# Kernel optimization log

Hardware: AMD Instinct MI355X
Metric: run time of the kernel (lower is better)

## Reference

```python
import jax, jax.numpy as jnp
import numpy as np
import math

H = 16          # num heads
D = 64          # head dim
MAX_POS = 512   # max_position_embeddings


def setup_inputs() -> dict:
    key = jax.random.key(0)
    ks = jax.random.split(key, 8)
    B, S, E = 8, 512, 1024
    scale = 1.0 / math.sqrt(E)
    return {
        "hidden_states": jax.random.normal(ks[0], (B, S, E), jnp.float32),
        "attention_mask": jnp.zeros((B, 1, 1, S), jnp.float32),
        "Wq": jax.random.normal(ks[1], (E, E), jnp.float32) * scale,
        "bq": jnp.zeros((E,), jnp.float32),
        "Wk": jax.random.normal(ks[2], (E, E), jnp.float32) * scale,
        "bk": jnp.zeros((E,), jnp.float32),
        "Wv": jax.random.normal(ks[3], (E, E), jnp.float32) * scale,
        "bv": jnp.zeros((E,), jnp.float32),
        "dist_emb": jax.random.normal(ks[4], (2 * MAX_POS - 1, D), jnp.float32) * 0.02,
    }


def reference(hidden_states, attention_mask, Wq, bq, Wk, bk, Wv, bv, dist_emb):
    B, S, E = hidden_states.shape

    def heads(x):  # [B,S,E] -> [B,H,S,D]
        return x.reshape(B, S, H, D).transpose(0, 2, 1, 3)

    q = heads(hidden_states @ Wq + bq)
    k = heads(hidden_states @ Wk + bk)
    v = heads(hidden_states @ Wv + bv)

    # raw scores [B,H,S,S]
    scores = jnp.einsum('bhld,bhrd->bhlr', q, k)

    # relative position embedding lookup: distance[l,r] = l - r
    pos = jnp.arange(S)
    distance = pos[:, None] - pos[None, :]               # [S,S]
    pe = dist_emb[distance + MAX_POS - 1]                # [S,S,D]
    scores = scores + jnp.einsum('bhld,lrd->bhlr', q, pe)
    scores = scores + jnp.einsum('bhrd,lrd->bhlr', k, pe)

    scores = scores / math.sqrt(D) + attention_mask
    probs = jax.nn.softmax(scores, axis=-1)

    ctx = jnp.einsum('bhlr,bhrd->bhld', probs, v)        # [B,H,S,D]
    ctx = ctx.transpose(0, 2, 1, 3).reshape(B, S, H * D)
    return ctx
```

## Files before the change

kernel.cpp:

```cpp
#include <hip/hip_runtime.h>

#define BATCH 8
#define SEQ   512
#define EMB   1024
#define NH    16
#define HD    64

typedef __bf16 bf16x8 __attribute__((ext_vector_type(8)));
typedef float  f32x4  __attribute__((ext_vector_type(4)));

__device__ __forceinline__ unsigned short f2bf(float f){
  union { float f; unsigned u; } v; v.f = f;
  unsigned r = v.u + 0x7FFFu + ((v.u >> 16) & 1u);
  return (unsigned short)(r >> 16);
}
__device__ __forceinline__ unsigned short f2bfr(float f){
  union { float f; unsigned u; } v; v.f = f;
  return (unsigned short)((v.u + 0x8000u) >> 16);
}
__device__ __forceinline__ float bf2f(unsigned short s){
  union { unsigned u; float f; } v; v.u = ((unsigned)s) << 16;
  return v.f;
}

__device__ __forceinline__ float dpp_max16(float x){
  int t;
  t = __builtin_amdgcn_update_dpp(0, __builtin_bit_cast(int, x), 0xB1, 0xF, 0xF, true);
  x = fmaxf(x, __builtin_bit_cast(float, t));
  t = __builtin_amdgcn_update_dpp(0, __builtin_bit_cast(int, x), 0x4E, 0xF, 0xF, true);
  x = fmaxf(x, __builtin_bit_cast(float, t));
  t = __builtin_amdgcn_update_dpp(0, __builtin_bit_cast(int, x), 0x141, 0xF, 0xF, true);
  x = fmaxf(x, __builtin_bit_cast(float, t));
  t = __builtin_amdgcn_update_dpp(0, __builtin_bit_cast(int, x), 0x140, 0xF, 0xF, true);
  x = fmaxf(x, __builtin_bit_cast(float, t));
  return x;
}
__device__ __forceinline__ float dpp_sum16(float x){
  int t;
  t = __builtin_amdgcn_update_dpp(0, __builtin_bit_cast(int, x), 0xB1, 0xF, 0xF, true);
  x += __builtin_bit_cast(float, t);
  t = __builtin_amdgcn_update_dpp(0, __builtin_bit_cast(int, x), 0x4E, 0xF, 0xF, true);
  x += __builtin_bit_cast(float, t);
  t = __builtin_amdgcn_update_dpp(0, __builtin_bit_cast(int, x), 0x141, 0xF, 0xF, true);
  x += __builtin_bit_cast(float, t);
  t = __builtin_amdgcn_update_dpp(0, __builtin_bit_cast(int, x), 0x140, 0xF, 0xF, true);
  x += __builtin_bit_cast(float, t);
  return x;
}

__device__ __forceinline__ int swzc(int row, int chunk){
  return row * 128 + (((chunk ^ (row & 7)) & 7) << 4);
}
__device__ __forceinline__ int swz2(int row, int col){
  return row * 128 + ((((col >> 3) ^ (row & 7)) & 7) << 4) + ((col & 7) << 1);
}

__device__ __forceinline__ void gload16(const unsigned short* g, unsigned char* lds){
  __builtin_amdgcn_global_load_lds((const __attribute__((address_space(1))) unsigned int*)g,
                                   (__attribute__((address_space(3))) unsigned int*)lds,
                                   16, 0, 0);
}

__global__ void k_prep(const float* __restrict__ hid, unsigned short* __restrict__ hidb,
                       const float* __restrict__ dist, unsigned short* __restrict__ distb){
  int bid = blockIdx.x;
  if (bid < 4096){
    int i = (bid * 256 + threadIdx.x) * 4;
    float4 v = *(const float4*)(hid + i);
    ushort4 o; o.x = f2bf(v.x); o.y = f2bf(v.y); o.z = f2bf(v.z); o.w = f2bf(v.w);
    *(ushort4*)(hidb + i) = o;
  } else {
    int i = (bid - 4096) * 256 + threadIdx.x;
    distb[i] = (i < 1023 * 64) ? f2bf(dist[i]) : (unsigned short)0;
  }
}

__global__ void k_wt3(const float* __restrict__ Wq, const float* __restrict__ Wk,
                      const float* __restrict__ Wv, unsigned short* __restrict__ wqt,
                      unsigned short* __restrict__ wkt, unsigned short* __restrict__ wvt){
  const float* W = (blockIdx.z == 0) ? Wq : (blockIdx.z == 1) ? Wk : Wv;
  unsigned short* WT = (blockIdx.z == 0) ? wqt : (blockIdx.z == 1) ? wkt : wvt;
  __shared__ float t[32][33];
  int n0 = blockIdx.x * 32, k0 = blockIdx.y * 32;
  int tx = threadIdx.x, ty = threadIdx.y;
#pragma unroll
  for (int i = 0; i < 4; i++)
    t[ty + 8*i][tx] = W[(k0 + ty + 8*i) * EMB + n0 + tx];
  __syncthreads();
#pragma unroll
  for (int i = 0; i < 4; i++)
    WT[(n0 + ty + 8*i) * EMB + k0 + tx] = f2bf(t[tx][ty + 8*i]);
}

__global__ __launch_bounds__(256, 3) void k_gemm3(const unsigned short* __restrict__ A,
                                                  const unsigned short* __restrict__ wqt,
                                                  const unsigned short* __restrict__ wkt,
                                                  const unsigned short* __restrict__ wvt,
                                                  const float* __restrict__ bq,
                                                  const float* __restrict__ bk,
                                                  const float* __restrict__ bv,
                                                  unsigned short* __restrict__ qb,
                                                  unsigned short* __restrict__ kb,
                                                  unsigned short* __restrict__ vtb){
  int z = blockIdx.z;
  const unsigned short* BT = (z == 0) ? wqt : (z == 1) ? wkt : wvt;
  const float* bias = (z == 0) ? bq : (z == 1) ? bk : bv;
  unsigned short* out = (z == 0) ? qb : (z == 1) ? kb : vtb;
  int mode = (z == 2);

  __shared__ __align__(16) unsigned char sA[128 * 128];
  __shared__ __align__(16) unsigned char sB[128 * 128];
  int m0 = blockIdx.y * 128, n0 = blockIdx.x * 128;
  int t = threadIdx.x, w = t >> 6, lane = t & 63, g = lane >> 4, lr = lane & 15;
  int rowbase = (w >> 1) * 64, colbase = (w & 1) * 64;
  int lrow = lane >> 3, lc = lane & 7;
  f32x4 acc[4][4] = {};
  for (int k0 = 0; k0 < EMB; k0 += 64){
    __syncthreads();
#pragma unroll
    for (int i = 0; i < 4; i++){
      int row = (w + 4*i) * 8 + lrow;
      int cg  = lc ^ (row & 7);
      gload16(A  + (m0 + row) * EMB + k0 + cg*8, sA + (w + 4*i) * 1024);
      gload16(BT + (n0 + row) * EMB + k0 + cg*8, sB + (w + 4*i) * 1024);
    }
    __syncthreads();
#pragma unroll
    for (int kk = 0; kk < 2; kk++){
      bf16x8 af[4], bfv[4];
#pragma unroll
      for (int i = 0; i < 4; i++) af[i]  = *(const bf16x8*)(sA + swzc(rowbase + 16*i + lr, kk*4 + g));
#pragma unroll
      for (int j = 0; j < 4; j++) bfv[j] = *(const bf16x8*)(sB + swzc(colbase + 16*j + lr, kk*4 + g));
#pragma unroll
      for (int i = 0; i < 4; i++)
#pragma unroll
        for (int j = 0; j < 4; j++)
          acc[i][j] = __builtin_amdgcn_mfma_f32_16x16x32_bf16(af[i], bfv[j], acc[i][j], 0, 0, 0);
    }
  }
#pragma unroll
  for (int i = 0; i < 4; i++)
#pragma unroll
    for (int j = 0; j < 4; j++)
#pragma unroll
      for (int r = 0; r < 4; r++){
        int m = m0 + rowbase + 16*i + 4*g + r;
        int n = n0 + colbase + 16*j + lr;
        float val = acc[i][j][r] + bias[n];
        int b = m >> 9, s = m & 511, h = n >> 6, d = n & 63;
        int idx = (mode == 0) ? (((b*NH + h)*SEQ + s)*HD + d)
                              : (((b*NH + h)*HD + d)*SEQ + s);
        out[idx] = f2bf(val);
      }
}

__global__ __launch_bounds__(256, 2) void k_attn(const unsigned short* __restrict__ qb,
                                                 const unsigned short* __restrict__ kb,
                                                 const unsigned short* __restrict__ vtb,
                                                 const unsigned short* __restrict__ distb,
                                                 const float* __restrict__ mask,
                                                 float* __restrict__ out){
  __shared__ __align__(16) unsigned char sK[2][64 * 128];
  __shared__ __align__(16) unsigned char sV[2][64 * 128];
  __shared__ __align__(16) unsigned char sSA[4][2624];
  __shared__ __align__(16) unsigned char sSB[4][2560];

  const float SCL  = 0.125f * 1.4426950408889634f;
  const float L2E  = 1.4426950408889634f;

  int bid = blockIdx.x;
  int wgid = (bid & 7) * 128 + (bid >> 3);
  int lt = wgid & 7, h = (wgid >> 3) & 15, b = wgid >> 7;
  int L0 = lt * 64;
  int bh = b * NH + h;
  int t = threadIdx.x, w = t >> 6, lane = t & 63, g = lane >> 4, lr = lane & 15;
  int lbase = 16 * w;
  unsigned char* mySA = sSA[w];
  unsigned char* mySB = sSB[w];
  unsigned char* myP  = mySA;
  const float* maskp = mask + b * SEQ;

  const unsigned short* qrow = qb + (bh * SEQ + L0 + lbase + lr) * HD + 8 * g;
  bf16x8 aq0 = *(const bf16x8*)qrow;
  bf16x8 aq1 = *(const bf16x8*)(qrow + 32);

  bf16x8 pe[5][2];
#define LOAD_PE(JB) do {                                                     \
    const unsigned short* _pb = distb + ((JB) + 16*w + lr) * HD + 8*g;       \
    _Pragma("unroll")                                                        \
    for (int _j = 0; _j < 5; _j++){                                          \
      pe[_j][0] = *(const bf16x8*)(_pb + _j*16*HD);                          \
      pe[_j][1] = *(const bf16x8*)(_pb + _j*16*HD + 32); }                   \
  } while(0)

  {
    const unsigned short* ks = kb  + bh * SEQ * HD;
    const unsigned short* vs = vtb + bh * HD * SEQ;
#pragma unroll
    for (int i = 0; i < 2; i++){
      int row = (w + 4*i) * 8 + (lane >> 3);
      int cg  = (lane & 7) ^ (row & 7);
      gload16(ks + row * HD  + cg*8, sK[0] + (w + 4*i) * 1024);
      gload16(vs + row * SEQ + cg*8, sV[0] + (w + 4*i) * 1024);
    }
    LOAD_PE(L0 + 448);
  }

  f32x4 o[4] = {};
  float mrun[4], srun[4];
#pragma unroll
  for (int r = 0; r < 4; r++){ mrun[r] = -1e30f; srun[r] = 0.f; }

  for (int rt = 0; rt < 8; rt++){
    int R0 = rt * 64;
    int cur = rt & 1;
    __syncthreads();

    if (rt < 7){
      const unsigned short* ks = kb  + (bh * SEQ + R0 + 64) * HD;
      const unsigned short* vs = vtb + bh * HD * SEQ + R0 + 64;
#pragma unroll
      for (int i = 0; i < 2; i++){
        int row = (w + 4*i) * 8 + (lane >> 3);
        int cg  = (lane & 7) ^ (row & 7);
        gload16(ks + row * HD  + cg*8, sK[cur ^ 1] + (w + 4*i) * 1024);
        gload16(vs + row * SEQ + cg*8, sV[cur ^ 1] + (w + 4*i) * 1024);
      }
    }

    float mreg[4];
#pragma unroll
    for (int f = 0; f < 4; f++) mreg[f] = maskp[R0 + 16*f + lr];

    __builtin_amdgcn_s_setprio(1);
    f32x4 sc[4];
#pragma unroll
    for (int f = 0; f < 4; f++){
      bf16x8 k0 = *(const bf16x8*)(sK[cur] + swzc(16*f + lr, g));
      bf16x8 k1 = *(const bf16x8*)(sK[cur] + swzc(16*f + lr, 4 + g));
      f32x4 a = {};
      a = __builtin_amdgcn_mfma_f32_16x16x32_bf16(aq0, k0, a, 0, 0, 0);
      a = __builtin_amdgcn_mfma_f32_16x16x32_bf16(aq1, k1, a, 0, 0, 0);
      sc[f] = a;
      f32x4 b0 = {}, b1 = {};
      b0 = __builtin_amdgcn_mfma_f32_16x16x32_bf16(k0, pe[3 - f][0], b0, 0, 0, 0);
      b0 = __builtin_amdgcn_mfma_f32_16x16x32_bf16(k1, pe[3 - f][1], b0, 0, 0, 0);
      b1 = __builtin_amdgcn_mfma_f32_16x16x32_bf16(k0, pe[4 - f][0], b1, 0, 0, 0);
      b1 = __builtin_amdgcn_mfma_f32_16x16x32_bf16(k1, pe[4 - f][1], b1, 0, 0, 0);
#pragma unroll
      for (int reg = 0; reg < 4; reg++){
        int ss = 4*g + reg + lr;
        float v = (ss >= 15) ? b0[reg] : b1[reg];
        int row = 16*f + 4*g + reg;
        int col = (ss + 1) & 15;
        *(unsigned short*)(mySB + row*40 + col*2) = f2bfr(v);
      }
    }

#pragma unroll
    for (int jt2 = 0; jt2 < 5; jt2++){
      f32x4 a = {};
      a = __builtin_amdgcn_mfma_f32_16x16x32_bf16(aq0, pe[jt2][0], a, 0, 0, 0);
      a = __builtin_amdgcn_mfma_f32_16x16x32_bf16(aq1, pe[jt2][1], a, 0, 0, 0);
#pragma unroll
      for (int reg = 0; reg < 4; reg++){
        int rloc = 63 + 4*g + reg - lr - 16*jt2;
        int addr = ((unsigned)rloc < 64u) ? (rloc*40 + (4*g + reg)*2) : 2560;
        *(unsigned short*)(mySA + addr) = f2bfr(a[reg]);
      }
    }
    __builtin_amdgcn_s_setprio(0);

    if (rt < 7) LOAD_PE(L0 + 448 - 64*(rt + 1));

#pragma unroll
    for (int f = 0; f < 4; f++){
      ushort4 sa = *(const ushort4*)(mySA + (16*f + lr)*40 + 8*g);
      ushort4 sb = *(const ushort4*)(mySB + (16*f + lr)*40 + 8*g);
      float madd = mreg[f] * L2E;
      sc[f][0] = (sc[f][0] + bf2f(sa.x) + bf2f(sb.x)) * SCL + madd;
      sc[f][1] = (sc[f][1] + bf2f(sa.y) + bf2f(sb.y)) * SCL + madd;
      sc[f][2] = (sc[f][2] + bf2f(sa.z) + bf2f(sb.z)) * SCL + madd;
      sc[f][3] = (sc[f][3] + bf2f(sa.w) + bf2f(sb.w)) * SCL + madd;
    }

    float fac[4];
#pragma unroll
    for (int r = 0; r < 4; r++){
      float tm = fmaxf(fmaxf(sc[0][r], sc[1][r]), fmaxf(sc[2][r], sc[3][r]));
      tm = dpp_max16(tm);
      float mnew = fmaxf(mrun[r], tm);
      float fr = exp2f(mrun[r] - mnew);
      float ps = 0.f;
#pragma unroll
      for (int f = 0; f < 4; f++){ float p = exp2f(sc[f][r] - mnew); sc[f][r] = p; ps += p; }
      ps = dpp_sum16(ps);
      srun[r] = srun[r] * fr + ps;
      mrun[r] = mnew;
      fac[r]  = fr;
    }
#pragma unroll
    for (int df = 0; df < 4; df++)
#pragma unroll
      for (int r = 0; r < 4; r++) o[df][r] *= fac[r];

#pragma unroll
    for (int f = 0; f < 4; f++)
#pragma unroll
      for (int r = 0; r < 4; r++)
        *(unsigned short*)(myP + swz2(4*g + r, 16*f + lr)) = f2bfr(sc[f][r]);

    __builtin_amdgcn_s_setprio(1);
#pragma unroll
    for (int kk = 0; kk < 2; kk++){
      bf16x8 pf = *(const bf16x8*)(myP + swzc(lr, kk*4 + g));
#pragma unroll
      for (int df = 0; df < 4; df++){
        bf16x8 vf = *(const bf16x8*)(sV[cur] + swzc(16*df + lr, kk*4 + g));
        o[df] = __builtin_amdgcn_mfma_f32_16x16x32_bf16(pf, vf, o[df], 0, 0, 0);
      }
    }
    __builtin_amdgcn_s_setprio(0);
  }

#pragma unroll
  for (int r = 0; r < 4; r++){
    float inv = 1.0f / srun[r];
#pragma unroll
    for (int df = 0; df < 4; df++){
      int l = L0 + lbase + 4*g + r;
      out[(b * SEQ + l) * EMB + h * HD + 16*df + lr] = o[df][r] * inv;
    }
  }
#undef LOAD_PE
}

extern "C" void kernel_launch(void* const* d_in, const int* in_sizes, int n_in,
                              void* d_out, int out_size, void* d_ws, size_t ws_size,
                              hipStream_t stream) {
  (void)in_sizes; (void)n_in; (void)out_size; (void)ws_size;
  const float* hid  = (const float*)d_in[0];
  const float* mask = (const float*)d_in[1];
  const float* Wq   = (const float*)d_in[2];
  const float* bq   = (const float*)d_in[3];
  const float* Wk   = (const float*)d_in[4];
  const float* bk   = (const float*)d_in[5];
  const float* Wv   = (const float*)d_in[6];
  const float* bv   = (const float*)d_in[7];
  const float* dist = (const float*)d_in[8];
  float* out = (float*)d_out;

  unsigned char* ws = (unsigned char*)d_ws;
  unsigned short* hidb  = (unsigned short*)ws;
  unsigned short* wqt   = hidb + 4096 * 1024;
  unsigned short* wkt   = wqt  + 1024 * 1024;
  unsigned short* wvt   = wkt  + 1024 * 1024;
  unsigned short* distb = wvt  + 1024 * 1024;
  unsigned short* qb    = distb + 1024 * 64;
  unsigned short* kb    = qb + BATCH * NH * SEQ * HD;
  unsigned short* vtb   = kb + BATCH * NH * SEQ * HD;

  k_prep<<<4352, 256, 0, stream>>>(hid, hidb, dist, distb);
  k_wt3<<<dim3(32, 32, 3), dim3(32, 8), 0, stream>>>(Wq, Wk, Wv, wqt, wkt, wvt);
  k_gemm3<<<dim3(8, 32, 3), 256, 0, stream>>>(hidb, wqt, wkt, wvt, bq, bk, bv, qb, kb, vtb);
  k_attn<<<1024, 256, 0, stream>>>(qb, kb, vtb, distb, mask, out);
}
```

Baseline: 109.1 us.

## Stage K/V tiles through registers into a single LDS buffer

The attention kernel stops double-buffering K and V tiles in LDS with direct global-to-LDS loads. Each tile is now prefetched into registers, written to one shared LDS buffer after a barrier, and the next tile's global loads are issued before a second barrier. This halves LDS use for K/V, which may help occupancy, at the cost of two barriers per iteration, extra registers, and VGPR round-trips instead of async LDS loads.

```diff
diff --git a/kernel.cpp b/kernel.cpp
--- a/kernel.cpp
+++ b/kernel.cpp
@@ -59,6 +59,11 @@
   __builtin_amdgcn_global_load_lds((const __attribute__((address_space(1))) unsigned int*)g,
                                    (__attribute__((address_space(3))) unsigned int*)lds,
                                    16, 0, 0);
+}
+
+__device__ __forceinline__ void bar_lds(){
+  asm volatile("s_waitcnt lgkmcnt(0)" ::: "memory");
+  __builtin_amdgcn_s_barrier();
 }
 
 __global__ void k_prep(const float* __restrict__ hid, unsigned short* __restrict__ hidb,
@@ -161,8 +166,8 @@
                                                  const unsigned short* __restrict__ distb,
                                                  const float* __restrict__ mask,
                                                  float* __restrict__ out){
-  __shared__ __align__(16) unsigned char sK[2][64 * 128];
-  __shared__ __align__(16) unsigned char sV[2][64 * 128];
+  __shared__ __align__(16) unsigned char sK[64 * 128];
+  __shared__ __align__(16) unsigned char sV[64 * 128];
   __shared__ __align__(16) unsigned char sSA[4][2624];
   __shared__ __align__(16) unsigned char sSB[4][2560];
 
@@ -194,18 +199,17 @@
       pe[_j][1] = *(const bf16x8*)(_pb + _j*16*HD + 32); }                   \
   } while(0)
 
-  {
-    const unsigned short* ks = kb  + bh * SEQ * HD;
-    const unsigned short* vs = vtb + bh * HD * SEQ;
-#pragma unroll
-    for (int i = 0; i < 2; i++){
-      int row = (w + 4*i) * 8 + (lane >> 3);
-      int cg  = (lane & 7) ^ (row & 7);
-      gload16(ks + row * HD  + cg*8, sK[0] + (w + 4*i) * 1024);
-      gload16(vs + row * SEQ + cg*8, sV[0] + (w + 4*i) * 1024);
-    }
-    LOAD_PE(L0 + 448);
-  }
+  int lrow = lane >> 3, lc = lane & 7;
+  int row0 = w * 8 + lrow,      row1 = (w + 4) * 8 + lrow;
+  int cg0  = lc ^ (row0 & 7),   cg1  = lc ^ (row1 & 7);
+  const unsigned short* kbase = kb  + bh * SEQ * HD;
+  const unsigned short* vbase = vtb + bh * HD * SEQ;
+
+  uint4 kst0 = *(const uint4*)(kbase + row0 * HD  + cg0 * 8);
+  uint4 kst1 = *(const uint4*)(kbase + row1 * HD  + cg1 * 8);
+  uint4 vst0 = *(const uint4*)(vbase + row0 * SEQ + cg0 * 8);
+  uint4 vst1 = *(const uint4*)(vbase + row1 * SEQ + cg1 * 8);
+  LOAD_PE(L0 + 448);
 
   f32x4 o[4] = {};
   float mrun[4], srun[4];
@@ -214,20 +218,24 @@
 
   for (int rt = 0; rt < 8; rt++){
     int R0 = rt * 64;
-    int cur = rt & 1;
-    __syncthreads();
+
+    bar_lds();
+
+    *(uint4*)(sK + w * 1024 + lane * 16)       = kst0;
+    *(uint4*)(sK + (w + 4) * 1024 + lane * 16) = kst1;
+    *(uint4*)(sV + w * 1024 + lane * 16)       = vst0;
+    *(uint4*)(sV + (w + 4) * 1024 + lane * 16) = vst1;
 
     if (rt < 7){
-      const unsigned short* ks = kb  + (bh * SEQ + R0 + 64) * HD;
-      const unsigned short* vs = vtb + bh * HD * SEQ + R0 + 64;
-#pragma unroll
-      for (int i = 0; i < 2; i++){
-        int row = (w + 4*i) * 8 + (lane >> 3);
-        int cg  = (lane & 7) ^ (row & 7);
-        gload16(ks + row * HD  + cg*8, sK[cur ^ 1] + (w + 4*i) * 1024);
-        gload16(vs + row * SEQ + cg*8, sV[cur ^ 1] + (w + 4*i) * 1024);
-      }
-    }
+      const unsigned short* ks = kbase + (R0 + 64) * HD;
+      const unsigned short* vs = vbase + (R0 + 64);
+      kst0 = *(const uint4*)(ks + row0 * HD  + cg0 * 8);
+      kst1 = *(const uint4*)(ks + row1 * HD  + cg1 * 8);
+      vst0 = *(const uint4*)(vs + row0 * SEQ + cg0 * 8);
+      vst1 = *(const uint4*)(vs + row1 * SEQ + cg1 * 8);
+    }
+
+    bar_lds();
 
     float mreg[4];
 #pragma unroll
@@ -237,8 +245,8 @@
     f32x4 sc[4];
 #pragma unroll
     for (int f = 0; f < 4; f++){
-      bf16x8 k0 = *(const bf16x8*)(sK[cur] + swzc(16*f + lr, g));
-      bf16x8 k1 = *(const bf16x8*)(sK[cur] + swzc(16*f + lr, 4 + g));
+      bf16x8 k0 = *(const bf16x8*)(sK + swzc(16*f + lr, g));
+      bf16x8 k1 = *(const bf16x8*)(sK + swzc(16*f + lr, 4 + g));
       f32x4 a = {};
       a = __builtin_amdgcn_mfma_f32_16x16x32_bf16(aq0, k0, a, 0, 0, 0);
       a = __builtin_amdgcn_mfma_f32_16x16x32_bf16(aq1, k1, a, 0, 0, 0);
@@ -317,7 +325,7 @@
       bf16x8 pf = *(const bf16x8*)(myP + swzc(lr, kk*4 + g));
 #pragma unroll
       for (int df = 0; df < 4; df++){
-        bf16x8 vf = *(const bf16x8*)(sV[cur] + swzc(16*df + lr, kk*4 + g));
+        bf16x8 vf = *(const bf16x8*)(sV + swzc(16*df + lr, kk*4 + g));
         o[df] = __builtin_amdgcn_mfma_f32_16x16x32_bf16(pf, vf, o[df], 0, 0, 0);
       }
     }
```

New measurement: 104.3 us. 4.4% less time.
